# Optimization experiments

Measured on AMD Instinct MI355X. Metric: run time of the kernel, lower is better.

The kernel has to match this reference:

```python
import jax, jax.numpy as jnp
import numpy as np

NUM_BINS = 15
GAMMA_INITIAL = 1.0
EPS = 1e-20


def setup_inputs() -> dict:
    key = jax.random.key(0)
    k1, k2 = jax.random.split(key)
    N, C = 1048576, 128
    inp = jax.random.normal(k1, (N, C), dtype=jnp.float32)
    target = jax.random.randint(k2, (N,), 0, C, dtype=jnp.int64)
    # bin_stats from __init__: bin i covers [i/num_bins, (i+1)/num_bins), gamma=gamma_initial
    bin_uppers = (jnp.arange(1, NUM_BINS, dtype=jnp.float32) / NUM_BINS)  # interior boundaries [num_bins-1]
    gammas = jnp.full((NUM_BINS,), GAMMA_INITIAL, dtype=jnp.float32)
    return {"input": inp, "target": target, "bin_uppers": bin_uppers, "gammas": gammas}


def reference(input, target, bin_uppers, gammas):
    # [N, C] logits -> per-sample logpt at target class
    logp = jax.nn.log_softmax(input, axis=1)                       # [N, C]
    logpt = jnp.take_along_axis(logp, target[:, None], axis=1)[:, 0]  # [N]
    pt = jnp.exp(logpt)                                            # [N]
    # vectorized replacement of the Python bin-search: pt in [lower, upper) -> bin index
    # (first bin catches pt < uppers[0], last bin catches pt >= uppers[-1])
    bin_idx = jnp.searchsorted(bin_uppers, pt, side="right")       # [N] in [0, num_bins-1]
    gamma = gammas[bin_idx]                                        # [N] (gamma lookup, detached in original)
    gamma_sign = jnp.sign(gamma)
    gamma_mag = jnp.abs(gamma)
    loss = -((1.0 - gamma_sign * pt + EPS) ** gamma_mag) * logpt
    return loss.sum()
```

## Files before the change

kernel.cpp:

```cpp
#include <hip/hip_runtime.h>

#define NBINS 15

__device__ __forceinline__ float rdlane_f(float v, int lane) {
    return __int_as_float(__builtin_amdgcn_readlane(__float_as_int(v), lane));
}

__global__ __launch_bounds__(256) void adafocal_partial(
    const float* __restrict__ inp,
    const int* __restrict__ target,
    const float* __restrict__ bin_uppers,
    const float* __restrict__ gammas,
    float* __restrict__ partial,
    int N)
{
    __shared__ float  s_g[NBINS];
    __shared__ float2 s_coll[4][128];
    __shared__ float  s_wsum[4];

    if (threadIdx.x < NBINS) s_g[threadIdx.x] = gammas[threadIdx.x];
    __syncthreads();

    float u[NBINS - 1];
    #pragma unroll
    for (int i = 0; i < NBINS - 1; ++i) u[i] = bin_uppers[i];

    const int lane  = threadIdx.x & 63;
    const int half  = lane >> 5;
    const int wid   = threadIdx.x >> 6;
    const int gwave = blockIdx.x * 4 + wid;
    const int wrow0 = gwave * 128;

    s_coll[wid][lane]      = make_float2(1.0f, 0.0f);
    s_coll[wid][64 + lane] = make_float2(1.0f, 0.0f);

    int2 tt = make_int2(0, 0);
    if (wrow0 + 2 * lane + 1 < N)      tt = ((const int2*)target)[(wrow0 >> 1) + lane];
    else if (wrow0 + 2 * lane < N)     tt.x = target[wrow0 + 2 * lane];

    #pragma unroll
    for (int h = 0; h < 2; ++h) {
        #pragma unroll 8
        for (int k = 0; k < 32; ++k) {
            const int grow = wrow0 + 64 * h + 2 * k;
            if (grow >= N) continue;
            const bool full = (grow + 1 < N);

            float4 v = make_float4(0.f, 0.f, 0.f, 0.f);
            if (full || lane < 32)
                v = *(const float4*)(inp + (size_t)grow * 128 + (lane << 2));

            float e = __expf(v.x) + __expf(v.y) + __expf(v.z) + __expf(v.w);
            #pragma unroll
            for (int m = 1; m < 32; m <<= 1)
                e += __shfl_xor(e, m, 32);

            const int t0 = __builtin_amdgcn_readlane(tt.x, 32 * h + k);
            const int t1 = __builtin_amdgcn_readlane(tt.y, 32 * h + k);

            const float a0  = (t0 & 1) ? v.y : v.x;
            const float b0  = (t0 & 1) ? v.w : v.z;
            const float xt0 = rdlane_f((t0 & 2) ? b0 : a0, t0 >> 2);
            const float a1  = (t1 & 1) ? v.y : v.x;
            const float b1  = (t1 & 1) ? v.w : v.z;
            const float xt1 = rdlane_f((t1 & 2) ? b1 : a1, 32 + (t1 >> 2));

            float2 val;
            val.x = e;
            val.y = (lane == 0) ? xt0 : xt1;
            if (lane == 0 || (full && lane == 32))
                s_coll[wid][64 * h + 2 * k + half] = val;
        }
    }

    float acc = 0.0f;
    #pragma unroll
    for (int h = 0; h < 2; ++h) {
        const float2 cv   = s_coll[wid][64 * h + lane];
        const float logpt = cv.y - __logf(cv.x);
        const float pt    = __expf(logpt);

        int b = 0;
        #pragma unroll
        for (int i = 0; i < NBINS - 1; ++i)
            b += (u[i] <= pt) ? 1 : 0;

        const float g     = s_g[b];
        const float gsign = (g > 0.0f) ? 1.0f : (g < 0.0f ? -1.0f : 0.0f);
        const float gmag  = fabsf(g);
        const float base  = 1.0f - gsign * pt + 1e-20f;
        const float powv  = (gmag == 1.0f) ? base : __powf(base, gmag);
        acc -= powv * logpt;
    }

    #pragma unroll
    for (int m = 1; m < 64; m <<= 1)
        acc += __shfl_xor(acc, m);
    if (lane == 0) s_wsum[wid] = acc;
    __syncthreads();
    if (threadIdx.x == 0)
        partial[blockIdx.x] = (s_wsum[0] + s_wsum[1]) + (s_wsum[2] + s_wsum[3]);
}

__global__ __launch_bounds__(256) void adafocal_final(
    const float* __restrict__ partial, float* __restrict__ out, int nblocks)
{
    __shared__ float s_wsum[4];
    float acc = 0.0f;
    for (int i = threadIdx.x; i < nblocks; i += 256) acc += partial[i];
    #pragma unroll
    for (int m = 1; m < 64; m <<= 1)
        acc += __shfl_xor(acc, m);
    const int lane = threadIdx.x & 63;
    const int wid  = threadIdx.x >> 6;
    if (lane == 0) s_wsum[wid] = acc;
    __syncthreads();
    if (threadIdx.x == 0)
        out[0] = (s_wsum[0] + s_wsum[1]) + (s_wsum[2] + s_wsum[3]);
}

extern "C" void kernel_launch(void* const* d_in, const int* in_sizes, int n_in,
                              void* d_out, int out_size, void* d_ws, size_t ws_size,
                              hipStream_t stream) {
    const float* inp        = (const float*)d_in[0];
    const int*   targetp    = (const int*)d_in[1];
    const float* bin_uppers = (const float*)d_in[2];
    const float* gammas     = (const float*)d_in[3];
    float* out = (float*)d_out;

    const int N = in_sizes[1];
    const int nwaves  = (N + 127) / 128;
    const int nblocks = (nwaves + 3) / 4;

    float* partial = (float*)d_ws;

    adafocal_partial<<<nblocks, 256, 0, stream>>>(inp, targetp, bin_uppers, gammas, partial, N);
    adafocal_final<<<1, 256, 0, stream>>>(partial, out, nblocks);
}
```

Measured before the change: 107.1 us.

## Use DPP row reductions, nontemporal loads, and a bounds-free fast path

Replaces the 32-lane shuffle-xor reduction with a DPP row_shr and row_bcast sequence, so the sum lands in lanes 31 and 63, which then write to shared memory. Splits the loop into a full-tile fast path with no bounds checks that uses nontemporal float4 loads, and a guarded tail path for the last partial tile. The aim is to cut the ds_swizzle/permute cost of the reduction and the per-iteration branch overhead, and to avoid polluting the cache with streamed input. It adds code size and relies on the DPP semantics being correct.

```diff
diff --git a/kernel.cpp b/kernel.cpp
--- a/kernel.cpp
+++ b/kernel.cpp
@@ -2,8 +2,25 @@
 
 #define NBINS 15
 
+typedef float f32x4 __attribute__((ext_vector_type(4)));
+
 __device__ __forceinline__ float rdlane_f(float v, int lane) {
     return __int_as_float(__builtin_amdgcn_readlane(__float_as_int(v), lane));
+}
+
+template <int CTRL, int RMASK>
+__device__ __forceinline__ float dpp_add(float e) {
+    int moved = __builtin_amdgcn_update_dpp(0, __float_as_int(e), CTRL, RMASK, 0xf, true);
+    return e + __int_as_float(moved);
+}
+
+__device__ __forceinline__ float half32_sum(float e) {
+    e = dpp_add<0x111, 0xf>(e);
+    e = dpp_add<0x112, 0xf>(e);
+    e = dpp_add<0x114, 0xf>(e);
+    e = dpp_add<0x118, 0xf>(e);
+    e = dpp_add<0x142, 0xa>(e);
+    return e;
 }
 
 __global__ __launch_bounds__(256) void adafocal_partial(
@@ -26,38 +43,25 @@
     for (int i = 0; i < NBINS - 1; ++i) u[i] = bin_uppers[i];
 
     const int lane  = threadIdx.x & 63;
-    const int half  = lane >> 5;
     const int wid   = threadIdx.x >> 6;
     const int gwave = blockIdx.x * 4 + wid;
     const int wrow0 = gwave * 128;
-
-    s_coll[wid][lane]      = make_float2(1.0f, 0.0f);
-    s_coll[wid][64 + lane] = make_float2(1.0f, 0.0f);
 
     int2 tt = make_int2(0, 0);
     if (wrow0 + 2 * lane + 1 < N)      tt = ((const int2*)target)[(wrow0 >> 1) + lane];
     else if (wrow0 + 2 * lane < N)     tt.x = target[wrow0 + 2 * lane];
 
-    #pragma unroll
-    for (int h = 0; h < 2; ++h) {
-        #pragma unroll 8
-        for (int k = 0; k < 32; ++k) {
-            const int grow = wrow0 + 64 * h + 2 * k;
-            if (grow >= N) continue;
-            const bool full = (grow + 1 < N);
-
-            float4 v = make_float4(0.f, 0.f, 0.f, 0.f);
-            if (full || lane < 32)
-                v = *(const float4*)(inp + (size_t)grow * 128 + (lane << 2));
+    if (wrow0 + 128 <= N) {
+        #pragma unroll 4
+        for (int k = 0; k < 64; ++k) {
+            const f32x4 v = __builtin_nontemporal_load(
+                (const f32x4*)(inp + (size_t)(wrow0 + 2 * k) * 128) + lane);
 
             float e = __expf(v.x) + __expf(v.y) + __expf(v.z) + __expf(v.w);
-            #pragma unroll
-            for (int m = 1; m < 32; m <<= 1)
-                e += __shfl_xor(e, m, 32);
+            e = half32_sum(e);
 
-            const int t0 = __builtin_amdgcn_readlane(tt.x, 32 * h + k);
-            const int t1 = __builtin_amdgcn_readlane(tt.y, 32 * h + k);
-
+            const int t0 = __builtin_amdgcn_readlane(tt.x, k);
+            const int t1 = __builtin_amdgcn_readlane(tt.y, k);
             const float a0  = (t0 & 1) ? v.y : v.x;
             const float b0  = (t0 & 1) ? v.w : v.z;
             const float xt0 = rdlane_f((t0 & 2) ? b0 : a0, t0 >> 2);
@@ -67,9 +71,35 @@
 
             float2 val;
             val.x = e;
-            val.y = (lane == 0) ? xt0 : xt1;
-            if (lane == 0 || (full && lane == 32))
-                s_coll[wid][64 * h + 2 * k + half] = val;
+            val.y = (lane < 32) ? xt0 : xt1;
+            if ((lane & 31) == 31)
+                s_coll[wid][2 * k + (lane >> 5)] = val;
+        }
+    } else {
+        s_coll[wid][lane]      = make_float2(1.0f, 0.0f);
+        s_coll[wid][64 + lane] = make_float2(1.0f, 0.0f);
+        for (int k = 0; k < 64; ++k) {
+            const int grow = wrow0 + 2 * k;
+            if (grow >= N) break;
+            const bool full = (grow + 1 < N);
+            f32x4 v = {0.f, 0.f, 0.f, 0.f};
+            if (full || lane < 32)
+                v = *((const f32x4*)(inp + (size_t)grow * 128) + lane);
+            float e = __expf(v.x) + __expf(v.y) + __expf(v.z) + __expf(v.w);
+            e = half32_sum(e);
+            const int t0 = __builtin_amdgcn_readlane(tt.x, k);
+            const int t1 = __builtin_amdgcn_readlane(tt.y, k);
+            const float a0  = (t0 & 1) ? v.y : v.x;
+            const float b0  = (t0 & 1) ? v.w : v.z;
+            const float xt0 = rdlane_f((t0 & 2) ? b0 : a0, t0 >> 2);
+            const float a1  = (t1 & 1) ? v.y : v.x;
+            const float b1  = (t1 & 1) ? v.w : v.z;
+            const float xt1 = rdlane_f((t1 & 2) ? b1 : a1, 32 + (t1 >> 2));
+            float2 val;
+            val.x = e;
+            val.y = (lane < 32) ? xt0 : xt1;
+            if (lane == 31 || (full && lane == 63))
+                s_coll[wid][2 * k + (lane >> 5)] = val;
         }
     }
 
```

After: 95.48 us. -10.8%, faster.
